# Performance work log

Measured on AMD Instinct MI355X. Metric: run time of the kernel, lower is better.

Reference implementation:

```python
import jax, jax.numpy as jnp
import numpy as np

B, N, DIM = 2, 4096, 1024
HEADS, DH = 16, 64
W = 512                       # window_size; look_backward=1, look_forward=0 (causal)
INNER = HEADS * DH            # 1024
FF_INNER = int(DIM * 4 * 2 / 3)  # 2730, GEGLU inner dim
MASK_VAL = -1e9


def setup_inputs() -> dict:
    key = jax.random.key(0)
    ks = jax.random.split(key, 6)
    s = 0.02
    return {
        "x": jax.random.normal(ks[0], (B, N, DIM), jnp.float32),
        "mask": jnp.ones((B, N), jnp.bool_),
        "ln1_w": jnp.ones((DIM,), jnp.float32),
        "ln1_b": jnp.zeros((DIM,), jnp.float32),
        "w_qkv": jax.random.normal(ks[1], (DIM, 3 * INNER), jnp.float32) * s,
        "w_out": jax.random.normal(ks[2], (INNER, DIM), jnp.float32) * s,
        "ln2_w": jnp.ones((DIM,), jnp.float32),
        "ln2_b": jnp.zeros((DIM,), jnp.float32),
        "w_ff1": jax.random.normal(ks[3], (DIM, 2 * FF_INNER), jnp.float32) * s,
        "w_ff2": jax.random.normal(ks[4], (FF_INNER, DIM), jnp.float32) * s,
    }


def layer_norm(x, w, b, eps=1e-5):
    mu = x.mean(-1, keepdims=True)
    var = ((x - mu) ** 2).mean(-1, keepdims=True)
    return (x - mu) * jax.lax.rsqrt(var + eps) * w + b


def look_around(t, pad_value):
    # t: (..., nw, w, ...) over axis=-3/-2 layout (b?, nw, w, d?) handled by caller.
    # prepend previous window along the window axis (axis=-3 for 5D k/v, axis=0 for positions)
    return t


def local_attention(q, k, v, mask):
    # q,k,v: [b, h, n, d]; causal sliding-window attention, look_backward=1,
    # exact_windowsize=True (each query sees exactly the previous W positions + itself).
    b, h, n, d = q.shape
    nw = n // W
    scale = d ** -0.5
    qw = q.reshape(b, h, nw, W, d) * scale
    kw = k.reshape(b, h, nw, W, d)
    vw = v.reshape(b, h, nw, W, d)

    # look_around: concat previous window (zeros for window 0) -> keys of size 2W
    def prev(t):
        return jnp.pad(t, ((0, 0), (0, 0), (1, 0), (0, 0), (0, 0)))[:, :, :-1]
    k2 = jnp.concatenate([prev(kw), kw], axis=3)  # [b,h,nw,2W,d]
    v2 = jnp.concatenate([prev(vw), vw], axis=3)

    # absolute positions; pad windows get index -1
    t_pos = jnp.arange(n).reshape(nw, W)
    t_prev = jnp.pad(t_pos, ((1, 0), (0, 0)), constant_values=-1)[:-1]
    bq_t = t_pos                                  # [nw, W]
    bk_t = jnp.concatenate([t_prev, t_pos], axis=-1)  # [nw, 2W]

    pad_mask = bk_t == -1                                       # [nw,2W]
    causal_mask = bq_t[:, :, None] < bk_t[:, None, :]           # key after query
    exact_mask = bq_t[:, :, None] > (bk_t[:, None, :] + W)      # beyond window (look_backward*W)
    invalid = pad_mask[:, None, :] | causal_mask | exact_mask   # [nw,W,2W]

    # key padding mask from input mask
    mw = mask.reshape(b, nw, W)
    m_prev = jnp.pad(mw, ((0, 0), (1, 0), (0, 0)), constant_values=False)[:, :-1]
    mk = jnp.concatenate([m_prev, mw], axis=-1)                 # [b,nw,2W]

    sim = jnp.einsum('bhnid,bhnjd->bhnij', qw, k2)              # [b,h,nw,W,2W]
    bad = invalid[None, None] | (~mk)[:, None, :, None, :]
    sim = jnp.where(bad, MASK_VAL, sim)
    attn = jax.nn.softmax(sim, axis=-1)
    out = jnp.einsum('bhnij,bhnjd->bhnid', attn, v2)
    return out.reshape(b, h, n, d)


def reference(x, mask, ln1_w, ln1_b, w_qkv, w_out, ln2_w, ln2_b, w_ff1, w_ff2):
    b, n, _ = x.shape
    # ---- LocalMHA (prenorm) ----
    h = layer_norm(x, ln1_w, ln1_b)
    qkv = h @ w_qkv                                   # [b,n,3*inner]
    q, k, v = jnp.split(qkv, 3, axis=-1)
    def to_heads(t):
        return t.reshape(b, n, HEADS, DH).transpose(0, 2, 1, 3)  # b h n d
    q, k, v = to_heads(q), to_heads(k), to_heads(v)
    o = local_attention(q, k, v, mask)
    o = o.transpose(0, 2, 1, 3).reshape(b, n, INNER)
    x = x + o @ w_out
    # ---- GEGLU FeedForward (prenorm via LayerNorm in Sequential) ----
    h2 = layer_norm(x, ln2_w, ln2_b)
    u = h2 @ w_ff1
    a, gate = jnp.split(u, 2, axis=-1)
    ff = (a * jax.nn.gelu(gate, approximate=False)) @ w_ff2
    return x + ff
```

## Files before the change

### kernel.cpp

```cpp
#include <hip/hip_runtime.h>
#include <cstdint>


#define DEVI __device__ __forceinline__

typedef __bf16 bf16x8 __attribute__((ext_vector_type(8)));
typedef float f32x4 __attribute__((ext_vector_type(4)));

typedef __attribute__((address_space(1))) void gvoid_t;
typedef __attribute__((address_space(3))) void lvoid_t;

DEVI void gld16(const void* g, void* l) {
  __builtin_amdgcn_global_load_lds((gvoid_t*)g, (lvoid_t*)l, 16, 0, 0);
}

DEVI unsigned short f2bf(float f) {
  union { float f; unsigned int u; } c; c.f = f;
  unsigned int u = c.u;
  return (unsigned short)((u + 0x7fffu + ((u >> 16) & 1u)) >> 16);
}

DEVI float fexp2(float x) {
#if __has_builtin(__builtin_amdgcn_exp2f)
  return __builtin_amdgcn_exp2f(x);
#else
  return exp2f(x);
#endif
}

DEVI f32x4 mfma16(bf16x8 a, bf16x8 b, f32x4 c) {
  return __builtin_amdgcn_mfma_f32_16x16x32_bf16(a, b, c, 0, 0, 0);
}

__global__ __launch_bounds__(256) void wtrans_all_k(
    const float* __restrict__ wqkv, const float* __restrict__ wout,
    const float* __restrict__ wff1, const float* __restrict__ wff2,
    unsigned short* __restrict__ wT_qkv, unsigned short* __restrict__ wT_out,
    unsigned short* __restrict__ wTa, unsigned short* __restrict__ wTg,
    unsigned short* __restrict__ wT_ff2)
{
  __shared__ float tile[32][33];
  int idx = blockIdx.x;
  const float* W; unsigned short* WT;
  int K, strideW, colOff, Ncols, KC, kb, nb;
  if (idx < 3072) {
    W = wqkv; WT = wT_qkv; K = 1024; strideW = 3072; colOff = 0; Ncols = 3072; KC = 1024;
    kb = (idx & 31) * 32; nb = (idx >> 5) * 32;
  } else if (idx < 4096) {
    idx -= 3072;
    W = wout; WT = wT_out; K = 1024; strideW = 1024; colOff = 0; Ncols = 1024; KC = 1024;
    kb = (idx & 31) * 32; nb = (idx >> 5) * 32;
  } else if (idx < 6912) {
    idx -= 4096;
    W = wff1; WT = wTa; K = 1024; strideW = 5460; colOff = 0; Ncols = 2730; KC = 1024;
    kb = (idx & 31) * 32; nb = (idx >> 5) * 32;
  } else if (idx < 9728) {
    idx -= 6912;
    W = wff1; WT = wTg; K = 1024; strideW = 5460; colOff = 2730; Ncols = 2730; KC = 1024;
    kb = (idx & 31) * 32; nb = (idx >> 5) * 32;
  } else {
    idx -= 9728;
    W = wff2; WT = wT_ff2; K = 2730; strideW = 1024; colOff = 0; Ncols = 1024; KC = 2816;
    kb = (idx % 88) * 32; nb = (idx / 88) * 32;
  }
  const int tx = threadIdx.x & 31, ty = threadIdx.x >> 5;
#pragma unroll
  for (int i = 0; i < 4; ++i) {
    const int k = kb + ty + i * 8, n = nb + tx;
    float v = 0.f;
    if (k < K && n < Ncols) v = W[(size_t)k * strideW + colOff + n];
    tile[ty + i * 8][tx] = v;
  }
  __syncthreads();
#pragma unroll
  for (int i = 0; i < 4; ++i) {
    const int n = nb + ty + i * 8, k = kb + tx;
    WT[(size_t)n * KC + k] = f2bf(tile[tx][ty + i * 8]);
  }
}

__global__ __launch_bounds__(256) void ln_k(
    const float* __restrict__ x, const float* __restrict__ w,
    const float* __restrict__ b, unsigned short* __restrict__ out)
{
  const int wid = threadIdx.x >> 6, lane = threadIdx.x & 63;
  const int row = blockIdx.x * 4 + wid;
  const float* xr = x + (size_t)row * 1024;
  float v[16];
  float s = 0.f;
#pragma unroll
  for (int i = 0; i < 16; ++i) { v[i] = xr[lane + i * 64]; s += v[i]; }
#pragma unroll
  for (int off = 32; off > 0; off >>= 1) s += __shfl_xor(s, off, 64);
  const float mu = s * (1.f / 1024.f);
  float s2 = 0.f;
#pragma unroll
  for (int i = 0; i < 16; ++i) { const float d = v[i] - mu; s2 += d * d; }
#pragma unroll
  for (int off = 32; off > 0; off >>= 1) s2 += __shfl_xor(s2, off, 64);
  const float rs = rsqrtf(s2 * (1.f / 1024.f) + 1e-5f);
#pragma unroll
  for (int i = 0; i < 16; ++i) {
    const int c = lane + i * 64;
    out[(size_t)row * 1024 + c] = f2bf((v[i] - mu) * rs * w[c] + b[c]);
  }
}

template <int EPI>
__global__ __launch_bounds__(256, 3) void gemm_k(
    const unsigned short* __restrict__ A, const unsigned short* __restrict__ BT,
    const float* __restrict__ resid, void* __restrict__ outp,
    unsigned short* __restrict__ vTp, int M, int N, int K)
{
  __shared__ __attribute__((aligned(16))) unsigned short Asm[128 * 64];
  __shared__ __attribute__((aligned(16))) unsigned short Bsm[128 * 64];
  const int tid = threadIdx.x;
  const int wid = tid >> 6, lane = tid & 63;
  const int wy = wid >> 1, wx = wid & 1;
  const int lr = lane & 15, quad = lane >> 4;
  const int lx = lr & 7;
  const int m0 = blockIdx.y * 128, n0 = blockIdx.x * 128;

  const unsigned short* pA[4];
  const unsigned short* pB[4];
#pragma unroll
  for (int iss = 0; iss < 4; ++iss) {
    const int ch = iss * 256 + wid * 64 + lane;
    const int row = ch >> 3;
    const int kcs = (ch & 7) ^ (row & 7);
    pA[iss] = &A[(size_t)(m0 + row) * K + kcs * 8];
    pB[iss] = &BT[(size_t)(n0 + row) * K + kcs * 8];
  }

  f32x4 acc[4][4] = {};

  for (int kit = 0; kit < (K >> 6); ++kit) {
    __syncthreads();
#pragma unroll
    for (int iss = 0; iss < 4; ++iss) {
      const int ldsoff = (iss * 256 + wid * 64) * 8;
      gld16(pA[iss], &Asm[ldsoff]);
      gld16(pB[iss], &Bsm[ldsoff]);
      pA[iss] += 64; pB[iss] += 64;
    }
    __syncthreads();

#pragma unroll
    for (int ks = 0; ks < 2; ++ks) {
      const int cph = (ks * 4 + quad) ^ lx;
      bf16x8 af[4], bfr[4];
#pragma unroll
      for (int t = 0; t < 4; ++t) {
        af[t]  = *(const bf16x8*)&Asm[(wy * 64 + t * 16 + lr) * 64 + cph * 8];
        bfr[t] = *(const bf16x8*)&Bsm[(wx * 64 + t * 16 + lr) * 64 + cph * 8];
      }
#pragma unroll
      for (int mt = 0; mt < 4; ++mt)
#pragma unroll
        for (int nt = 0; nt < 4; ++nt)
          acc[mt][nt] = mfma16(af[mt], bfr[nt], acc[mt][nt]);
    }
  }

  if (EPI == 0 && n0 >= 2048) {
    const int bb = m0 >> 12;
    const int tb = (m0 & 4095) + wy * 64;
#pragma unroll
    for (int mt = 0; mt < 4; ++mt)
#pragma unroll
      for (int nt = 0; nt < 4; ++nt) {
        const int c2 = n0 - 2048 + wx * 64 + nt * 16 + lr;
        const int t0 = tb + mt * 16 + quad * 4;
        union { unsigned short u[4]; uint2 v; } pk;
#pragma unroll
        for (int r = 0; r < 4; ++r) pk.u[r] = f2bf(acc[mt][nt][r]);
        *(uint2*)&vTp[(size_t)(bb * 1024 + c2) * 4096 + t0] = pk.v;
      }
    return;
  }

#pragma unroll
  for (int mt = 0; mt < 4; ++mt)
#pragma unroll
    for (int nt = 0; nt < 4; ++nt)
#pragma unroll
      for (int r = 0; r < 4; ++r) {
        const int row = m0 + wy * 64 + mt * 16 + quad * 4 + r;
        const int col = n0 + wx * 64 + nt * 16 + lr;
        if (EPI == 0) {
          ((unsigned short*)outp)[(size_t)row * 2048 + col] = f2bf(acc[mt][nt][r]);
        } else {
          const size_t idx = (size_t)row * N + col;
          ((float*)outp)[idx] = acc[mt][nt][r] + resid[idx];
        }
      }
}

__global__ __launch_bounds__(256, 3) void geglu_k(
    const unsigned short* __restrict__ A, const unsigned short* __restrict__ BTa,
    const unsigned short* __restrict__ BTg, unsigned short* __restrict__ outp,
    int M, int N, int K)
{
  __shared__ __attribute__((aligned(16))) unsigned short S[16384];
  const int tid = threadIdx.x;
  const int wid = tid >> 6, lane = tid & 63;
  const int wy = wid >> 1, wx = wid & 1;
  const int lr = lane & 15, quad = lane >> 4;
  const int lx = lr & 7;
  const int m0 = blockIdx.y * 128, n0 = blockIdx.x * 64;

  const unsigned short* pS[8];
#pragma unroll
  for (int iss = 0; iss < 8; ++iss) {
    const int ch = iss * 256 + wid * 64 + lane;
    if (ch < 1024) {
      const int row = ch >> 3, kcs = (ch & 7) ^ (row & 7);
      pS[iss] = &A[(size_t)(m0 + row) * K + kcs * 8];
    } else if (ch < 1536) {
      const int c = ch - 1024, row = c >> 3, kcs = (c & 7) ^ (row & 7);
      pS[iss] = &BTa[(size_t)(n0 + row) * K + kcs * 8];
    } else {
      const int c = ch - 1536, row = c >> 3, kcs = (c & 7) ^ (row & 7);
      pS[iss] = &BTg[(size_t)(n0 + row) * K + kcs * 8];
    }
  }

  f32x4 acc_a[4][2] = {};
  f32x4 acc_g[4][2] = {};

  for (int kit = 0; kit < (K >> 6); ++kit) {
    __syncthreads();
#pragma unroll
    for (int iss = 0; iss < 8; ++iss) {
      const int ldsoff = (iss * 256 + wid * 64) * 8;
      gld16(pS[iss], &S[ldsoff]);
      pS[iss] += 64;
    }
    __syncthreads();

#pragma unroll
    for (int ks = 0; ks < 2; ++ks) {
      const int cph = (ks * 4 + quad) ^ lx;
      bf16x8 af[4], ba[2], bg[2];
#pragma unroll
      for (int t = 0; t < 4; ++t)
        af[t] = *(const bf16x8*)&S[(wy * 64 + t * 16 + lr) * 64 + cph * 8];
#pragma unroll
      for (int t = 0; t < 2; ++t) {
        ba[t] = *(const bf16x8*)&S[8192 + (wx * 32 + t * 16 + lr) * 64 + cph * 8];
        bg[t] = *(const bf16x8*)&S[12288 + (wx * 32 + t * 16 + lr) * 64 + cph * 8];
      }
#pragma unroll
      for (int mt = 0; mt < 4; ++mt)
#pragma unroll
        for (int nt = 0; nt < 2; ++nt) {
          acc_a[mt][nt] = mfma16(af[mt], ba[nt], acc_a[mt][nt]);
          acc_g[mt][nt] = mfma16(af[mt], bg[nt], acc_g[mt][nt]);
        }
    }
  }

#pragma unroll
  for (int mt = 0; mt < 4; ++mt)
#pragma unroll
    for (int nt = 0; nt < 2; ++nt)
#pragma unroll
      for (int r = 0; r < 4; ++r) {
        const int row = m0 + wy * 64 + mt * 16 + quad * 4 + r;
        const int col = n0 + wx * 32 + nt * 16 + lr;
        const float a = acc_a[mt][nt][r];
        const float g = acc_g[mt][nt][r];
        const float ge = 0.5f * g * (1.0f + erff(g * 0.70710678118654752f));
        outp[(size_t)row * N + col] = f2bf(a * ge);
      }
}

__global__ __launch_bounds__(64, 2) void attn_k(
    const unsigned short* __restrict__ qk, const unsigned short* __restrict__ vT,
    unsigned short* __restrict__ o)
{
  __shared__ __attribute__((aligned(16))) unsigned short Ksm[64 * 64];
  __shared__ __attribute__((aligned(16))) unsigned short Vsm[64 * 64];
  __shared__ __attribute__((aligned(16))) unsigned short Psm[64 * 72];

  const int bx = blockIdx.x;
  const int qt = bx & 63, hh = (bx >> 6) & 15, b = bx >> 10;
  const int bhead = bx >> 6;
  const int lane = threadIdx.x & 63;
  const int lr = lane & 15, quad = lane >> 4;
  const int lx = lr & 7;
  const int q0 = qt * 64;
  const size_t rowB = (size_t)b * 4096;
  const float scale2 = 0.18033688011112042f;
  const int r8 = lane >> 3;
  const int c8 = (lane & 7) ^ (r8 & 7);

  bf16x8 qf[4][2];
#pragma unroll
  for (int mt = 0; mt < 4; ++mt)
#pragma unroll
    for (int ks = 0; ks < 2; ++ks)
      qf[mt][ks] = *(const bf16x8*)
          &qk[(rowB + q0 + mt * 16 + lr) * 2048 + hh * 64 + ks * 32 + quad * 8];

  f32x4 O[4][4] = {};
  float lS[4][4] = {};

  const int kstart = (q0 >= 512) ? (q0 - 512) : 0;
  const int ntiles = (q0 + 64 - kstart) >> 6;

  for (int kt = 0; kt < ntiles; ++kt) {
    const int k0t = kstart + kt * 64;
    __syncthreads();
#pragma unroll
    for (int i = 0; i < 8; ++i) {
      gld16(&qk[(rowB + k0t + i * 8 + r8) * 2048 + 1024 + hh * 64 + c8 * 8],
            &Ksm[i * 512]);
      gld16(&vT[((size_t)(bhead * 64 + i * 8 + r8)) * 4096 + k0t + c8 * 8],
            &Vsm[i * 512]);
    }
    __syncthreads();

    f32x4 S[4][4];
    bf16x8 kf[4][2];
#pragma unroll
    for (int nt = 0; nt < 4; ++nt)
#pragma unroll
      for (int ks = 0; ks < 2; ++ks)
        kf[nt][ks] = *(const bf16x8*)&Ksm[(nt * 16 + lr) * 64 + (((ks * 4 + quad) ^ lx)) * 8];
#pragma unroll
    for (int mt = 0; mt < 4; ++mt)
#pragma unroll
      for (int nt = 0; nt < 4; ++nt) {
        f32x4 z = {};
        z = mfma16(qf[mt][0], kf[nt][0], z);
        S[mt][nt] = mfma16(qf[mt][1], kf[nt][1], z);
      }

#pragma unroll
    for (int mt = 0; mt < 4; ++mt)
#pragma unroll
      for (int nt = 0; nt < 4; ++nt)
#pragma unroll
        for (int r = 0; r < 4; ++r) {
          const int qpos = q0 + mt * 16 + quad * 4 + r;
          const int kpos = k0t + nt * 16 + lr;
          const bool bad = (kpos > qpos) || (kpos < qpos - 512);
          const float p = bad ? 0.f : fexp2(S[mt][nt][r] * scale2);
          lS[mt][r] += p;
          Psm[(mt * 16 + quad * 4 + r) * 72 + nt * 16 + lr] = f2bf(p);
        }

    bf16x8 vf[4][2];
#pragma unroll
    for (int dt = 0; dt < 4; ++dt)
#pragma unroll
      for (int jt = 0; jt < 2; ++jt)
        vf[dt][jt] = *(const bf16x8*)&Vsm[(dt * 16 + lr) * 64 + (((jt * 4 + quad) ^ lx)) * 8];
#pragma unroll
    for (int mt = 0; mt < 4; ++mt)
#pragma unroll
      for (int jt = 0; jt < 2; ++jt) {
        const bf16x8 pf = *(const bf16x8*)&Psm[(mt * 16 + lr) * 72 + jt * 32 + quad * 8];
#pragma unroll
        for (int dt = 0; dt < 4; ++dt)
          O[mt][dt] = mfma16(pf, vf[dt][jt], O[mt][dt]);
      }
  }

#pragma unroll
  for (int mt = 0; mt < 4; ++mt)
#pragma unroll
    for (int r = 0; r < 4; ++r) {
      float s = lS[mt][r];
#pragma unroll
      for (int off = 1; off < 16; off <<= 1) s += __shfl_xor(s, off, 64);
      lS[mt][r] = 1.f / s;
    }

#pragma unroll
  for (int mt = 0; mt < 4; ++mt)
#pragma unroll
    for (int dt = 0; dt < 4; ++dt)
#pragma unroll
      for (int r = 0; r < 4; ++r) {
        const int row = q0 + mt * 16 + quad * 4 + r;
        o[(rowB + row) * 1024 + hh * 64 + dt * 16 + lr] = f2bf(O[mt][dt][r] * lS[mt][r]);
      }
}

extern "C" void kernel_launch(void* const* d_in, const int* in_sizes, int n_in,
                              void* d_out, int out_size, void* d_ws, size_t ws_size,
                              hipStream_t stream)
{
  (void)in_sizes; (void)n_in; (void)out_size; (void)ws_size;
  const float* x    = (const float*)d_in[0];
  const float* ln1w = (const float*)d_in[2];
  const float* ln1b = (const float*)d_in[3];
  const float* wqkv = (const float*)d_in[4];
  const float* wout = (const float*)d_in[5];
  const float* ln2w = (const float*)d_in[6];
  const float* ln2b = (const float*)d_in[7];
  const float* wff1 = (const float*)d_in[8];
  const float* wff2 = (const float*)d_in[9];

  char* p = (char*)d_ws;
  auto alloc = [&](size_t n) { char* r = p; p += (n + 255) & ~(size_t)255; return r; };
  unsigned short* wT_qkv = (unsigned short*)alloc(3072ull * 1024 * 2);
  unsigned short* wT_out = (unsigned short*)alloc(1024ull * 1024 * 2);
  unsigned short* wTa    = (unsigned short*)alloc(2816ull * 1024 * 2);
  unsigned short* wTg    = (unsigned short*)alloc(2816ull * 1024 * 2);
  unsigned short* wT_ff2 = (unsigned short*)alloc(1024ull * 2816 * 2);
  unsigned short* bufX   = (unsigned short*)alloc(8192ull * 1024 * 2);
  unsigned short* qkg    = (unsigned short*)alloc(8192ull * 3072 * 2);
  unsigned short* obuf   = (unsigned short*)alloc(8192ull * 1024 * 2);
  float*          x1     = (float*)alloc(8192ull * 1024 * 4);
  unsigned short* vT     = (unsigned short*)x1;

  wtrans_all_k<<<dim3(12544), 256, 0, stream>>>(wqkv, wout, wff1, wff2,
                                                wT_qkv, wT_out, wTa, wTg, wT_ff2);
  ln_k<<<dim3(2048), 256, 0, stream>>>(x, ln1w, ln1b, bufX);
  gemm_k<0><<<dim3(24, 64), 256, 0, stream>>>(bufX, wT_qkv, nullptr,
                                              (void*)qkg, vT, 8192, 3072, 1024);
  attn_k<<<dim3(2048), 64, 0, stream>>>(qkg, vT, obuf);
  gemm_k<1><<<dim3(8, 64), 256, 0, stream>>>(obuf, wT_out, x,
                                             (void*)x1, nullptr, 8192, 1024, 1024);
  ln_k<<<dim3(2048), 256, 0, stream>>>(x1, ln2w, ln2b, bufX);
  geglu_k<<<dim3(44, 64), 256, 0, stream>>>(bufX, wTa, wTg, qkg, 8192, 2816, 1024);
  gemm_k<1><<<dim3(8, 64), 256, 0, stream>>>(qkg, wT_ff2, x1,
                                             d_out, nullptr, 8192, 1024, 2816);
}
```

Measured before the change: 487.3 us.

## Fuse LN1 into weight transpose, stage V-transpose via LDS, load attention K/V directly

```diff
diff --git a/kernel.cpp b/kernel.cpp
--- a/kernel.cpp
+++ b/kernel.cpp
@@ -32,15 +32,41 @@
   return __builtin_amdgcn_mfma_f32_16x16x32_bf16(a, b, c, 0, 0, 0);
 }
 
-__global__ __launch_bounds__(256) void wtrans_all_k(
+__global__ __launch_bounds__(256) void wtrans_ln_k(
     const float* __restrict__ wqkv, const float* __restrict__ wout,
     const float* __restrict__ wff1, const float* __restrict__ wff2,
     unsigned short* __restrict__ wT_qkv, unsigned short* __restrict__ wT_out,
     unsigned short* __restrict__ wTa, unsigned short* __restrict__ wTg,
-    unsigned short* __restrict__ wT_ff2)
+    unsigned short* __restrict__ wT_ff2,
+    const float* __restrict__ x, const float* __restrict__ lnw,
+    const float* __restrict__ lnb, unsigned short* __restrict__ lnout)
 {
   __shared__ float tile[32][33];
   int idx = blockIdx.x;
+  if (idx >= 12544) {
+    const int wid = threadIdx.x >> 6, lane = threadIdx.x & 63;
+    const int row = (idx - 12544) * 4 + wid;
+    const float* xr = x + (size_t)row * 1024;
+    float v[16];
+    float s = 0.f;
+#pragma unroll
+    for (int i = 0; i < 16; ++i) { v[i] = xr[lane + i * 64]; s += v[i]; }
+#pragma unroll
+    for (int off = 32; off > 0; off >>= 1) s += __shfl_xor(s, off, 64);
+    const float mu = s * (1.f / 1024.f);
+    float s2 = 0.f;
+#pragma unroll
+    for (int i = 0; i < 16; ++i) { const float d = v[i] - mu; s2 += d * d; }
+#pragma unroll
+    for (int off = 32; off > 0; off >>= 1) s2 += __shfl_xor(s2, off, 64);
+    const float rs = rsqrtf(s2 * (1.f / 1024.f) + 1e-5f);
+#pragma unroll
+    for (int i = 0; i < 16; ++i) {
+      const int c = lane + i * 64;
+      lnout[(size_t)row * 1024 + c] = f2bf((v[i] - mu) * rs * lnw[c] + lnb[c]);
+    }
+    return;
+  }
   const float* W; unsigned short* WT;
   int K, strideW, colOff, Ncols, KC, kb, nb;
   if (idx < 3072) {
@@ -112,8 +138,7 @@
     const float* __restrict__ resid, void* __restrict__ outp,
     unsigned short* __restrict__ vTp, int M, int N, int K)
 {
-  __shared__ __attribute__((aligned(16))) unsigned short Asm[128 * 64];
-  __shared__ __attribute__((aligned(16))) unsigned short Bsm[128 * 64];
+  __shared__ __attribute__((aligned(16))) unsigned short S[(EPI == 0) ? 18432 : 16384];
   const int tid = threadIdx.x;
   const int wid = tid >> 6, lane = tid & 63;
   const int wy = wid >> 1, wx = wid & 1;
@@ -139,8 +164,8 @@
 #pragma unroll
     for (int iss = 0; iss < 4; ++iss) {
       const int ldsoff = (iss * 256 + wid * 64) * 8;
-      gld16(pA[iss], &Asm[ldsoff]);
-      gld16(pB[iss], &Bsm[ldsoff]);
+      gld16(pA[iss], &S[ldsoff]);
+      gld16(pB[iss], &S[8192 + ldsoff]);
       pA[iss] += 64; pB[iss] += 64;
     }
     __syncthreads();
@@ -151,8 +176,8 @@
       bf16x8 af[4], bfr[4];
 #pragma unroll
       for (int t = 0; t < 4; ++t) {
-        af[t]  = *(const bf16x8*)&Asm[(wy * 64 + t * 16 + lr) * 64 + cph * 8];
-        bfr[t] = *(const bf16x8*)&Bsm[(wx * 64 + t * 16 + lr) * 64 + cph * 8];
+        af[t]  = *(const bf16x8*)&S[(wy * 64 + t * 16 + lr) * 64 + cph * 8];
+        bfr[t] = *(const bf16x8*)&S[8192 + (wx * 64 + t * 16 + lr) * 64 + cph * 8];
       }
 #pragma unroll
       for (int mt = 0; mt < 4; ++mt)
@@ -163,19 +188,25 @@
   }
 
   if (EPI == 0 && n0 >= 2048) {
+    __syncthreads();
+    unsigned short* Wl = &S[wid * 4608];
+#pragma unroll
+    for (int mt = 0; mt < 4; ++mt)
+#pragma unroll
+      for (int nt = 0; nt < 4; ++nt) {
+        union { unsigned short u[4]; uint2 v; } pk;
+#pragma unroll
+        for (int r = 0; r < 4; ++r) pk.u[r] = f2bf(acc[mt][nt][r]);
+        *(uint2*)&Wl[(nt * 16 + lr) * 72 + mt * 16 + quad * 4] = pk.v;
+      }
     const int bb = m0 >> 12;
-    const int tb = (m0 & 4095) + wy * 64;
-#pragma unroll
-    for (int mt = 0; mt < 4; ++mt)
-#pragma unroll
-      for (int nt = 0; nt < 4; ++nt) {
-        const int c2 = n0 - 2048 + wx * 64 + nt * 16 + lr;
-        const int t0 = tb + mt * 16 + quad * 4;
-        union { unsigned short u[4]; uint2 v; } pk;
-#pragma unroll
-        for (int r = 0; r < 4; ++r) pk.u[r] = f2bf(acc[mt][nt][r]);
-        *(uint2*)&vTp[(size_t)(bb * 1024 + c2) * 4096 + t0] = pk.v;
-      }
+    const int t0 = (m0 & 4095) + wy * 64 + (lane & 7) * 8;
+    const int cbase = n0 - 2048 + wx * 64 + (lane >> 3);
+#pragma unroll
+    for (int p = 0; p < 8; ++p) {
+      const uint4 val = *(const uint4*)&Wl[(p * 8 + (lane >> 3)) * 72 + (lane & 7) * 8];
+      *(uint4*)&vTp[(size_t)(bb * 1024 + cbase + p * 8) * 4096 + t0] = val;
+    }
     return;
   }
 
@@ -279,8 +310,6 @@
     const unsigned short* __restrict__ qk, const unsigned short* __restrict__ vT,
     unsigned short* __restrict__ o)
 {
-  __shared__ __attribute__((aligned(16))) unsigned short Ksm[64 * 64];
-  __shared__ __attribute__((aligned(16))) unsigned short Vsm[64 * 64];
   __shared__ __attribute__((aligned(16))) unsigned short Psm[64 * 72];
 
   const int bx = blockIdx.x;
@@ -288,12 +317,9 @@
   const int bhead = bx >> 6;
   const int lane = threadIdx.x & 63;
   const int lr = lane & 15, quad = lane >> 4;
-  const int lx = lr & 7;
   const int q0 = qt * 64;
   const size_t rowB = (size_t)b * 4096;
   const float scale2 = 0.18033688011112042f;
-  const int r8 = lane >> 3;
-  const int c8 = (lane & 7) ^ (r8 & 7);
 
   bf16x8 qf[4][2];
 #pragma unroll
@@ -311,23 +337,16 @@
 
   for (int kt = 0; kt < ntiles; ++kt) {
     const int k0t = kstart + kt * 64;
-    __syncthreads();
-#pragma unroll
-    for (int i = 0; i < 8; ++i) {
-      gld16(&qk[(rowB + k0t + i * 8 + r8) * 2048 + 1024 + hh * 64 + c8 * 8],
-            &Ksm[i * 512]);
-      gld16(&vT[((size_t)(bhead * 64 + i * 8 + r8)) * 4096 + k0t + c8 * 8],
-            &Vsm[i * 512]);
-    }
-    __syncthreads();
+
+    bf16x8 kf[4][2];
+#pragma unroll
+    for (int nt = 0; nt < 4; ++nt)
+#pragma unroll
+      for (int ks = 0; ks < 2; ++ks)
+        kf[nt][ks] = *(const bf16x8*)
+            &qk[(rowB + k0t + nt * 16 + lr) * 2048 + 1024 + hh * 64 + ks * 32 + quad * 8];
 
     f32x4 S[4][4];
-    bf16x8 kf[4][2];
-#pragma unroll
-    for (int nt = 0; nt < 4; ++nt)
-#pragma unroll
-      for (int ks = 0; ks < 2; ++ks)
-        kf[nt][ks] = *(const bf16x8*)&Ksm[(nt * 16 + lr) * 64 + (((ks * 4 + quad) ^ lx)) * 8];
 #pragma unroll
     for (int mt = 0; mt < 4; ++mt)
 #pragma unroll
@@ -336,6 +355,14 @@
         z = mfma16(qf[mt][0], kf[nt][0], z);
         S[mt][nt] = mfma16(qf[mt][1], kf[nt][1], z);
       }
+
+    bf16x8 vf[4][2];
+#pragma unroll
+    for (int dt = 0; dt < 4; ++dt)
+#pragma unroll
+      for (int jt = 0; jt < 2; ++jt)
+        vf[dt][jt] = *(const bf16x8*)
+            &vT[((size_t)(bhead * 64 + dt * 16 + lr)) * 4096 + k0t + jt * 32 + quad * 8];
 
 #pragma unroll
     for (int mt = 0; mt < 4; ++mt)
@@ -351,12 +378,6 @@
           Psm[(mt * 16 + quad * 4 + r) * 72 + nt * 16 + lr] = f2bf(p);
         }
 
-    bf16x8 vf[4][2];
-#pragma unroll
-    for (int dt = 0; dt < 4; ++dt)
-#pragma unroll
-      for (int jt = 0; jt < 2; ++jt)
-        vf[dt][jt] = *(const bf16x8*)&Vsm[(dt * 16 + lr) * 64 + (((jt * 4 + quad) ^ lx)) * 8];
 #pragma unroll
     for (int mt = 0; mt < 4; ++mt)
 #pragma unroll
@@ -417,9 +438,9 @@
   float*          x1     = (float*)alloc(8192ull * 1024 * 4);
   unsigned short* vT     = (unsigned short*)x1;
 
-  wtrans_all_k<<<dim3(12544), 256, 0, stream>>>(wqkv, wout, wff1, wff2,
-                                                wT_qkv, wT_out, wTa, wTg, wT_ff2);
-  ln_k<<<dim3(2048), 256, 0, stream>>>(x, ln1w, ln1b, bufX);
+  wtrans_ln_k<<<dim3(14592), 256, 0, stream>>>(wqkv, wout, wff1, wff2,
+                                               wT_qkv, wT_out, wTa, wTg, wT_ff2,
+                                               x, ln1w, ln1b, bufX);
   gemm_k<0><<<dim3(24, 64), 256, 0, stream>>>(bufX, wT_qkv, nullptr,
                                               (void*)qkg, vT, 8192, 3072, 1024);
   attn_k<<<dim3(2048), 64, 0, stream>>>(qkg, vT, obuf);
```

Result: faster. 466.0 us (-4.4%).
